# Kernel optimization log

Measured on AMD Instinct MI355X. Metric: run time of the kernel, lower is better.

## Reference

```python
import jax, jax.numpy as jnp
import numpy as np

N_NODES = 50000
N_EDGES = 800000
D_IN = 128
HEADS = 4
D_OUT = 64
NEG_SLOPE = 0.2  # PyG GATConv default


def setup_inputs() -> dict:
    key = jax.random.key(0)
    ks = jax.random.split(key, 10)
    x = jax.random.normal(ks[0], (N_NODES, D_IN), dtype=jnp.float32)
    edge_index = jax.random.randint(ks[1], (2, N_EDGES), 0, N_NODES, dtype=jnp.int32)
    kg_labels = jax.random.randint(ks[2], (N_NODES,), 0, 32)
    kg_onehot = jax.nn.one_hot(kg_labels, 32, dtype=jnp.float32)
    s = 0.05
    W_gat = jax.random.normal(ks[3], (D_IN, HEADS * D_OUT), dtype=jnp.float32) * s
    att_src = jax.random.normal(ks[4], (HEADS, D_OUT), dtype=jnp.float32) * s
    att_dst = jax.random.normal(ks[5], (HEADS, D_OUT), dtype=jnp.float32) * s
    bias_gat = jax.random.normal(ks[6], (D_OUT,), dtype=jnp.float32) * s
    W_prior = jax.random.normal(ks[7], (32, D_OUT), dtype=jnp.float32) * s
    b_prior = jax.random.normal(ks[8], (D_OUT,), dtype=jnp.float32) * s
    gate = jnp.ones((1,), dtype=jnp.float32) * 0.5
    return {"x": x, "edge_index": edge_index, "kg_onehot": kg_onehot,
            "W_gat": W_gat, "att_src": att_src, "att_dst": att_dst,
            "bias_gat": bias_gat, "W_prior": W_prior, "b_prior": b_prior,
            "gate": gate}


def _gat_conv(x, edge_index, W_gat, att_src, att_dst, bias_gat):
    N = x.shape[0]
    H, F = att_src.shape
    # add self loops (PyG default add_self_loops=True)
    loops = jnp.arange(N, dtype=edge_index.dtype)
    src = jnp.concatenate([edge_index[0], loops])  # message source j
    dst = jnp.concatenate([edge_index[1], loops])  # aggregation target i
    h = (x @ W_gat).reshape(N, H, F)               # [N,H,F]
    a_src = jnp.sum(h * att_src[None], axis=-1)    # [N,H]
    a_dst = jnp.sum(h * att_dst[None], axis=-1)    # [N,H]
    alpha = jax.nn.leaky_relu(a_src[src] + a_dst[dst], NEG_SLOPE)  # [E,H]
    # segment softmax over destination neighborhoods
    amax = jax.ops.segment_max(alpha, dst, num_segments=N)
    amax = jnp.where(jnp.isfinite(amax), amax, 0.0)
    ex = jnp.exp(alpha - amax[dst])
    denom = jax.ops.segment_sum(ex, dst, num_segments=N)
    w = ex / (denom[dst] + 1e-16)                  # [E,H]
    # scatter-aggregate weighted source messages
    out = jax.ops.segment_sum(w[:, :, None] * h[src], dst, num_segments=N)  # [N,H,F]
    return out.mean(axis=1) + bias_gat             # concat=False -> mean heads


def reference(x, edge_index, kg_onehot, W_gat, att_src, att_dst, bias_gat,
              W_prior, b_prior, gate):
    x_gat = _gat_conv(x, edge_index, W_gat, att_src, att_dst, bias_gat)
    prior = kg_onehot @ W_prior + b_prior
    return (1.0 - gate) * x_gat + gate * prior
```

## Files before the change

kernel.cpp:

```cpp
#include <hip/hip_runtime.h>
#include <hip/hip_fp16.h>
#include <math.h>

#define N_NODES 50000
#define N_EDGES 800000
#define D_IN    128
#define HEADS   4
#define F       64
#define HF      256
#define NEG     0.2f
#define E_TOT   (N_EDGES + N_NODES)
#define GR      32
#define CHUNK   128
#define DSTRIDE 96

__global__ __launch_bounds__(256) void k_gemm(const float* __restrict__ x,
                                              const float* __restrict__ Wg,
                                              const float* __restrict__ att_src,
                                              const float* __restrict__ att_dst,
                                              __half* __restrict__ h,
                                              float* __restrict__ a8) {
    __shared__ float xs[D_IN][GR + 4];
    int row0 = blockIdx.x * GR;
    int tid = threadIdx.x;
    for (int i = tid; i < GR * D_IN; i += 256) {
        int r = i >> 7, c = i & 127;
        int gr = row0 + r;
        xs[c][r] = (gr < N_NODES) ? x[(size_t)gr * D_IN + c] : 0.f;
    }
    __syncthreads();
    int cg = tid & 127;
    int rh = tid >> 7;
    int c0 = cg * 2;
    float acc[16][2];
    #pragma unroll
    for (int r = 0; r < 16; ++r) { acc[r][0] = 0.f; acc[r][1] = 0.f; }
    #pragma unroll 2
    for (int k = 0; k < D_IN; ++k) {
        float2 w = *reinterpret_cast<const float2*>(&Wg[k * HF + c0]);
        const float4* xr = reinterpret_cast<const float4*>(&xs[k][rh * 16]);
        float xv[16];
        *reinterpret_cast<float4*>(&xv[0])  = xr[0];
        *reinterpret_cast<float4*>(&xv[4])  = xr[1];
        *reinterpret_cast<float4*>(&xv[8])  = xr[2];
        *reinterpret_cast<float4*>(&xv[12]) = xr[3];
        #pragma unroll
        for (int r = 0; r < 16; ++r) {
            acc[r][0] += xv[r] * w.x;
            acc[r][1] += xv[r] * w.y;
        }
    }
    #pragma unroll
    for (int r = 0; r < 16; ++r) {
        int gr = row0 + rh * 16 + r;
        if (gr < N_NODES)
            *reinterpret_cast<__half2*>(&h[(size_t)gr * HF + c0]) =
                __floats2half2_rn(acc[r][0], acc[r][1]);
    }
    int cl   = c0 & 63;
    int head = c0 >> 6;
    int lane = tid & 63;
    float As0 = att_src[head * F + cl], As1 = att_src[head * F + cl + 1];
    float Ad0 = att_dst[head * F + cl], Ad1 = att_dst[head * F + cl + 1];
    #pragma unroll
    for (int r = 0; r < 16; ++r) {
        float ps = acc[r][0] * As0 + acc[r][1] * As1;
        float pd = acc[r][0] * Ad0 + acc[r][1] * Ad1;
        #pragma unroll
        for (int off = 1; off <= 16; off <<= 1) {
            ps += __shfl_xor(ps, off, 64);
            pd += __shfl_xor(pd, off, 64);
        }
        if ((lane & 31) == 0) {
            int row = row0 + rh * 16 + r;
            if (row < N_NODES) {
                a8[row * 8 + head]     = ps;
                a8[row * 8 + 4 + head] = pd;
            }
        }
    }
}

__global__ void k_fill(const int* __restrict__ ei, int* __restrict__ deg,
                       int* __restrict__ csr) {
    int idx = blockIdx.x * blockDim.x + threadIdx.x;
    if (idx >= E_TOT) return;
    int src, dst;
    if (idx < N_EDGES) { src = ei[idx]; dst = ei[N_EDGES + idx]; }
    else               { src = dst = idx - N_EDGES; }
    int pos = atomicAdd(&deg[dst], 1);
    if (pos < DSTRIDE) csr[dst * DSTRIDE + pos] = src;
}

__global__ __launch_bounds__(256) void k_agg(
    const __half* __restrict__ h, const float* __restrict__ a8,
    const int* __restrict__ deg, const int* __restrict__ csr_src,
    const float* __restrict__ bias_gat, const float* __restrict__ onehot,
    const float* __restrict__ W_prior, const float* __restrict__ b_prior,
    const float* __restrict__ gate, float* __restrict__ out)
{
    __shared__ float wl[4][CHUNK * 4];
    __shared__ int   jl[4][CHUNK];
    int wv   = threadIdx.x >> 6;
    int lane = threadIdx.x & 63;
    int wid = (blockIdx.x << 2) + wv;
    if (wid >= N_NODES) return;
    const int i = wid;
    const int start = i * DSTRIDE;
    int cnt = deg[i];
    cnt = (cnt > DSTRIDE) ? DSTRIDE : cnt;
    const float4* a8v = reinterpret_cast<const float4*>(a8);
    const float4 ad = a8v[(size_t)i * 2 + 1];
    float g = gate[0];

    {
        float* wlw = wl[wv];
        int*   jlw = jl[wv];
        float al0[2][4];
        int jreg[2];
        float m[4] = {-INFINITY, -INFINITY, -INFINITY, -INFINITY};
        #pragma unroll
        for (int s2 = 0; s2 < 2; ++s2) {
            int e = s2 * 64 + lane;
            if (e < cnt) {
                int j = csr_src[start + e];
                jreg[s2] = j;
                float4 as = a8v[(size_t)j * 2];
                float a;
                a = as.x + ad.x; a = fmaxf(a, NEG * a); al0[s2][0] = a; m[0] = fmaxf(m[0], a);
                a = as.y + ad.y; a = fmaxf(a, NEG * a); al0[s2][1] = a; m[1] = fmaxf(m[1], a);
                a = as.z + ad.z; a = fmaxf(a, NEG * a); al0[s2][2] = a; m[2] = fmaxf(m[2], a);
                a = as.w + ad.w; a = fmaxf(a, NEG * a); al0[s2][3] = a; m[3] = fmaxf(m[3], a);
            }
        }
        #pragma unroll
        for (int off = 32; off; off >>= 1) {
            #pragma unroll
            for (int hh = 0; hh < 4; ++hh)
                m[hh] = fmaxf(m[hh], __shfl_xor(m[hh], off, 64));
        }
        float s[4] = {0.f, 0.f, 0.f, 0.f};
        #pragma unroll
        for (int s2 = 0; s2 < 2; ++s2) {
            int e = s2 * 64 + lane;
            if (e < cnt) {
                #pragma unroll
                for (int hh = 0; hh < 4; ++hh) {
                    float ex = __expf(al0[s2][hh] - m[hh]);
                    al0[s2][hh] = ex;
                    s[hh] += ex;
                }
            }
        }
        #pragma unroll
        for (int off = 32; off; off >>= 1) {
            #pragma unroll
            for (int hh = 0; hh < 4; ++hh)
                s[hh] += __shfl_xor(s[hh], off, 64);
        }
        float inv[4];
        #pragma unroll
        for (int hh = 0; hh < 4; ++hh) inv[hh] = 1.f / (s[hh] + 1e-16f);
        int ncp = (cnt + 7) & ~7;
        #pragma unroll
        for (int s2 = 0; s2 < 2; ++s2) {
            int e = s2 * 64 + lane;
            if (e < cnt) {
                *reinterpret_cast<float4*>(&wlw[e * 4]) =
                    make_float4(al0[s2][0] * inv[0], al0[s2][1] * inv[1],
                                al0[s2][2] * inv[2], al0[s2][3] * inv[3]);
                jlw[e] = jreg[s2];
            } else if (e < ncp) {
                *reinterpret_cast<float4*>(&wlw[e * 4]) = make_float4(0.f, 0.f, 0.f, 0.f);
                jlw[e] = 0;
            }
        }
        __builtin_amdgcn_wave_barrier();
        int hsel = lane >> 4;
        float4 acc = make_float4(0.f, 0.f, 0.f, 0.f);
        for (int t = 0; t < ncp; t += 8) {
            int4 jv0 = *reinterpret_cast<const int4*>(&jlw[t]);
            int4 jv1 = *reinterpret_cast<const int4*>(&jlw[t + 4]);
            #pragma unroll
            for (int k = 0; k < 8; ++k) {
                int j = (k < 4) ? ((const int*)&jv0)[k] : ((const int*)&jv1)[k - 4];
                float w = wlw[(t + k) * 4 + hsel];
                uint2 raw = *reinterpret_cast<const uint2*>(h + (size_t)j * HF + lane * 4);
                float2 f0 = __half22float2(*reinterpret_cast<const __half2*>(&raw.x));
                float2 f1 = __half22float2(*reinterpret_cast<const __half2*>(&raw.y));
                acc.x += w * f0.x; acc.y += w * f0.y;
                acc.z += w * f1.x; acc.w += w * f1.y;
            }
        }
        #pragma unroll
        for (int off = 16; off <= 32; off <<= 1) {
            acc.x += __shfl_xor(acc.x, off, 64);
            acc.y += __shfl_xor(acc.y, off, 64);
            acc.z += __shfl_xor(acc.z, off, 64);
            acc.w += __shfl_xor(acc.w, off, 64);
        }
        float ohv = (lane < 32) ? onehot[(size_t)i * 32 + lane] : 0.f;
        unsigned long long bm = __ballot(ohv != 0.f);
        int label = __ffsll(bm) - 1;
        if (hsel == 0) {
            int fo = lane & 15;
            float4 b4  = reinterpret_cast<const float4*>(bias_gat)[fo];
            float4 p4  = reinterpret_cast<const float4*>(W_prior + (size_t)label * F)[fo];
            float4 pb4 = reinterpret_cast<const float4*>(b_prior)[fo];
            float4 o;
            o.x = (1.f - g) * (acc.x * 0.25f + b4.x) + g * (p4.x + pb4.x);
            o.y = (1.f - g) * (acc.y * 0.25f + b4.y) + g * (p4.y + pb4.y);
            o.z = (1.f - g) * (acc.z * 0.25f + b4.z) + g * (p4.z + pb4.z);
            o.w = (1.f - g) * (acc.w * 0.25f + b4.w) + g * (p4.w + pb4.w);
            reinterpret_cast<float4*>(out + (size_t)i * F)[fo] = o;
        }
    }
}

extern "C" void kernel_launch(void* const* d_in, const int* in_sizes, int n_in,
                              void* d_out, int out_size, void* d_ws, size_t ws_size,
                              hipStream_t stream) {
    const float* x        = (const float*)d_in[0];
    const int*   ei       = (const int*)  d_in[1];
    const float* onehot   = (const float*)d_in[2];
    const float* Wg       = (const float*)d_in[3];
    const float* att_src  = (const float*)d_in[4];
    const float* att_dst  = (const float*)d_in[5];
    const float* bias_gat = (const float*)d_in[6];
    const float* W_prior  = (const float*)d_in[7];
    const float* b_prior  = (const float*)d_in[8];
    const float* gate     = (const float*)d_in[9];
    float* out = (float*)d_out;

    char* ws = (char*)d_ws;
    size_t off = 0;
    auto alloc = [&](size_t bytes) -> void* {
        void* p = ws + off;
        off = (off + bytes + 255) & ~(size_t)255;
        return p;
    };
    __half* h   = (__half*)alloc((size_t)N_NODES * HF * 2);
    float* a8   = (float*)alloc((size_t)N_NODES * 8 * 4);
    int*   deg  = (int*)  alloc(N_NODES * 4);
    int*   csr  = (int*)  alloc((size_t)N_NODES * DSTRIDE * 4);

    hipMemsetAsync(deg, 0, N_NODES * 4, stream);
    k_gemm<<<(N_NODES + GR - 1) / GR, 256, 0, stream>>>(x, Wg, att_src, att_dst, h, a8);
    k_fill<<<(E_TOT + 255) / 256, 256, 0, stream>>>(ei, deg, csr);
    k_agg <<<N_NODES / 4, 256, 0, stream>>>(h, a8, deg, csr,
                                            bias_gat, onehot, W_prior, b_prior,
                                            gate, out);
}
```

Before: 277.3 us.

## Use fp16 MFMA for node projection GEMM with LDS-staged output

Replaces the scalar fp32 FMA GEMM for x@W_gat with MFMA 16x16x32 f16 instructions, converting x and W tiles to half in shared memory. Output is staged in LDS for coalesced 16-byte stores, and attention logits are computed from the staged half values. The aim is to cut the GEMM's compute time. In exchange, inputs are rounded to fp16 before multiplication and the logits are computed from rounded h, so precision drops. W is re-converted per block on every K chunk.

```diff
diff --git a/kernel.cpp b/kernel.cpp
--- a/kernel.cpp
+++ b/kernel.cpp
@@ -14,69 +14,108 @@
 #define CHUNK   128
 #define DSTRIDE 96
 
+typedef _Float16 f16x8 __attribute__((ext_vector_type(8)));
+typedef float    f32x4 __attribute__((ext_vector_type(4)));
+
 __global__ __launch_bounds__(256) void k_gemm(const float* __restrict__ x,
                                               const float* __restrict__ Wg,
                                               const float* __restrict__ att_src,
                                               const float* __restrict__ att_dst,
                                               __half* __restrict__ h,
                                               float* __restrict__ a8) {
-    __shared__ float xs[D_IN][GR + 4];
-    int row0 = blockIdx.x * GR;
-    int tid = threadIdx.x;
-    for (int i = tid; i < GR * D_IN; i += 256) {
-        int r = i >> 7, c = i & 127;
-        int gr = row0 + r;
-        xs[c][r] = (gr < N_NODES) ? x[(size_t)gr * D_IN + c] : 0.f;
-    }
+    __shared__ __half xs[GR][136];
+    __shared__ __half wgt[HF][40];
+    __shared__ __half outs[GR][264];
+    const int tid  = threadIdx.x;
+    const int row0 = blockIdx.x * GR;
+
+    #pragma unroll
+    for (int i = 0; i < 4; ++i) {
+        int idx = tid + i * 256;
+        int r = idx >> 5, c4 = (idx & 31) * 4;
+        int grow = row0 + r;
+        float4 v = make_float4(0.f, 0.f, 0.f, 0.f);
+        if (grow < N_NODES) v = *reinterpret_cast<const float4*>(x + (size_t)grow * D_IN + c4);
+        __half2 p0 = __floats2half2_rn(v.x, v.y);
+        __half2 p1 = __floats2half2_rn(v.z, v.w);
+        *reinterpret_cast<__half2*>(&xs[r][c4])     = p0;
+        *reinterpret_cast<__half2*>(&xs[r][c4 + 2]) = p1;
+    }
+
+    const int wave = tid >> 6;
+    const int lane = tid & 63;
+    const int lrow = lane & 15;
+    const int lk8  = (lane >> 4) * 8;
+
+    f32x4 acc[2][4];
+    #pragma unroll
+    for (int mt = 0; mt < 2; ++mt)
+        #pragma unroll
+        for (int nt = 0; nt < 4; ++nt)
+            #pragma unroll
+            for (int r = 0; r < 4; ++r) acc[mt][nt][r] = 0.f;
+
+    for (int kc = 0; kc < 4; ++kc) {
+        if (kc > 0) __syncthreads();
+        #pragma unroll
+        for (int i = 0; i < 16; ++i) {
+            int p = tid + i * 256;
+            int n = p & 255, kp = p >> 8;
+            int k0 = kc * 32 + kp * 2;
+            float w0 = Wg[(size_t)k0 * HF + n];
+            float w1 = Wg[(size_t)(k0 + 1) * HF + n];
+            *reinterpret_cast<__half2*>(&wgt[n][kp * 2]) = __floats2half2_rn(w0, w1);
+        }
+        __syncthreads();
+        f16x8 a[2], b[4];
+        #pragma unroll
+        for (int mt = 0; mt < 2; ++mt)
+            a[mt] = *reinterpret_cast<const f16x8*>(&xs[mt * 16 + lrow][kc * 32 + lk8]);
+        #pragma unroll
+        for (int nt = 0; nt < 4; ++nt)
+            b[nt] = *reinterpret_cast<const f16x8*>(&wgt[wave * 64 + nt * 16 + lrow][lk8]);
+        #pragma unroll
+        for (int mt = 0; mt < 2; ++mt)
+            #pragma unroll
+            for (int nt = 0; nt < 4; ++nt)
+                acc[mt][nt] = __builtin_amdgcn_mfma_f32_16x16x32_f16(a[mt], b[nt], acc[mt][nt], 0, 0, 0);
+    }
+
+    #pragma unroll
+    for (int mt = 0; mt < 2; ++mt)
+        #pragma unroll
+        for (int nt = 0; nt < 4; ++nt) {
+            int col = wave * 64 + nt * 16 + (lane & 15);
+            int rb  = mt * 16 + (lane >> 4) * 4;
+            #pragma unroll
+            for (int r = 0; r < 4; ++r)
+                outs[rb + r][col] = __float2half_rn(acc[mt][nt][r]);
+        }
     __syncthreads();
-    int cg = tid & 127;
-    int rh = tid >> 7;
-    int c0 = cg * 2;
-    float acc[16][2];
-    #pragma unroll
-    for (int r = 0; r < 16; ++r) { acc[r][0] = 0.f; acc[r][1] = 0.f; }
-    #pragma unroll 2
-    for (int k = 0; k < D_IN; ++k) {
-        float2 w = *reinterpret_cast<const float2*>(&Wg[k * HF + c0]);
-        const float4* xr = reinterpret_cast<const float4*>(&xs[k][rh * 16]);
-        float xv[16];
-        *reinterpret_cast<float4*>(&xv[0])  = xr[0];
-        *reinterpret_cast<float4*>(&xv[4])  = xr[1];
-        *reinterpret_cast<float4*>(&xv[8])  = xr[2];
-        *reinterpret_cast<float4*>(&xv[12]) = xr[3];
-        #pragma unroll
-        for (int r = 0; r < 16; ++r) {
-            acc[r][0] += xv[r] * w.x;
-            acc[r][1] += xv[r] * w.y;
-        }
-    }
-    #pragma unroll
-    for (int r = 0; r < 16; ++r) {
-        int gr = row0 + rh * 16 + r;
-        if (gr < N_NODES)
-            *reinterpret_cast<__half2*>(&h[(size_t)gr * HF + c0]) =
-                __floats2half2_rn(acc[r][0], acc[r][1]);
-    }
-    int cl   = c0 & 63;
-    int head = c0 >> 6;
-    int lane = tid & 63;
-    float As0 = att_src[head * F + cl], As1 = att_src[head * F + cl + 1];
-    float Ad0 = att_dst[head * F + cl], Ad1 = att_dst[head * F + cl + 1];
-    #pragma unroll
-    for (int r = 0; r < 16; ++r) {
-        float ps = acc[r][0] * As0 + acc[r][1] * As1;
-        float pd = acc[r][0] * Ad0 + acc[r][1] * Ad1;
-        #pragma unroll
-        for (int off = 1; off <= 16; off <<= 1) {
-            ps += __shfl_xor(ps, off, 64);
-            pd += __shfl_xor(pd, off, 64);
-        }
-        if ((lane & 31) == 0) {
-            int row = row0 + rh * 16 + r;
-            if (row < N_NODES) {
-                a8[row * 8 + head]     = ps;
-                a8[row * 8 + 4 + head] = pd;
-            }
+    #pragma unroll
+    for (int i = 0; i < 4; ++i) {
+        int idx = tid + i * 256;
+        int r = idx >> 5, c8 = (idx & 31) * 8;
+        int grow = row0 + r;
+        if (grow < N_NODES) {
+            int4 v = *reinterpret_cast<const int4*>(&outs[r][c8]);
+            *reinterpret_cast<int4*>(h + (size_t)grow * HF + c8) = v;
+        }
+    }
+    {
+        int r = tid >> 3, which = tid & 7, head = which & 3;
+        int grow = row0 + r;
+        if (grow < N_NODES) {
+            const float* att = (which < 4) ? att_src : att_dst;
+            float dot = 0.f;
+            #pragma unroll
+            for (int f8 = 0; f8 < 8; ++f8) {
+                const __half* hp = &outs[r][head * F + f8 * 8];
+                #pragma unroll
+                for (int j = 0; j < 8; ++j)
+                    dot += __half2float(hp[j]) * att[head * F + f8 * 8 + j];
+            }
+            a8[(size_t)grow * 8 + which] = dot;
         }
     }
 }
```

New measurement: 235.8 us. 15.0% less time.
